# Kernel tuning notes

Hardware: AMD Instinct MI355X
Metric: run time of the kernel (lower is better)

Reference implementation:

```python
import jax, jax.numpy as jnp
import numpy as np

HEADS = 16
KV_HEADS = 4
DIM_HEAD = 64
DIM = 1024
B, N = 2, 2048


def setup_inputs() -> dict:
    key = jax.random.key(0)
    k1, k2, k3 = jax.random.split(key, 3)
    x = jax.random.normal(k1, (B, N, DIM), dtype=jnp.float32)
    Wq = jax.random.normal(k2, (DIM, HEADS * DIM_HEAD), dtype=jnp.float32) / np.sqrt(DIM)
    Wkv = jax.random.normal(k3, (DIM, 2 * KV_HEADS * DIM_HEAD), dtype=jnp.float32) / np.sqrt(DIM)
    k_scale = jnp.ones((HEADS, 1, DIM_HEAD), dtype=jnp.float32)
    return {"x": x, "Wq": Wq, "Wkv": Wkv, "k_scale": k_scale}


def reference(x, Wq, Wkv, k_scale):
    b, n, _ = x.shape
    g = HEADS // KV_HEADS  # query heads per kv head
    scale = DIM_HEAD ** -0.5
    # fused qkv projections (no bias)
    q = (x @ Wq).reshape(b, n, HEADS, DIM_HEAD)
    kv = x @ Wkv
    k, v = jnp.split(kv, 2, axis=-1)
    k = k.reshape(b, n, KV_HEADS, DIM_HEAD).transpose(0, 2, 1, 3)  # b k n d
    v = v.reshape(b, n, KV_HEADS, DIM_HEAD).transpose(0, 2, 1, 3)  # b k n d
    # group query heads: b, kv_heads, g, n, d
    qg = q.transpose(0, 2, 1, 3).reshape(b, KV_HEADS, g, n, DIM_HEAD)
    # per-query-head k scale, applied to the group-broadcast k (qk-norm)
    ks = k_scale.reshape(KV_HEADS, g, 1, DIM_HEAD)
    kk = k[:, :, None, :, :] * ks  # b k g n d
    dots = jnp.einsum('bkgid,bkgjd->bkgij', qg, kk) * scale
    attn = jax.nn.softmax(dots, axis=-1)
    out = jnp.einsum('bkgij,bkjd->bkgid', attn, v)  # v broadcast over g
    out = out.reshape(b, HEADS, n, DIM_HEAD).transpose(0, 2, 1, 3).reshape(b, n, HEADS * DIM_HEAD)
    return out
```

## Files before the change

### kernel.cpp

```cpp
#include <hip/hip_runtime.h>
#include <stdint.h>
#include <math.h>

typedef __attribute__((ext_vector_type(8))) __bf16 bf16x8;
typedef __attribute__((ext_vector_type(4))) float f32x4;
typedef __attribute__((ext_vector_type(16))) float f32x16;

__device__ __forceinline__ uint32_t f32_to_bf16_rne(float f) {
  union { float f; uint32_t u; } v; v.f = f;
  return (v.u + 0x7FFFu + ((v.u >> 16) & 1u)) >> 16;
}

__device__ __forceinline__ uint32_t cvt_pk_bf16(float lo, float hi) {
  uint32_t r;
  asm("v_cvt_pk_bf16_f32 %0, %1, %2" : "=v"(r) : "v"(lo), "v"(hi));
  return r;
}

__device__ __forceinline__ void gld16(void* lds, const void* g) {
  __builtin_amdgcn_global_load_lds(
      (__attribute__((address_space(1))) void*)(g),
      (__attribute__((address_space(3))) void*)(lds), 16, 0, 0);
}

__device__ __forceinline__ f32x4 mfma16(bf16x8 a, bf16x8 b, f32x4 c) {
  return __builtin_amdgcn_mfma_f32_16x16x32_bf16(a, b, c, 0, 0, 0);
}
__device__ __forceinline__ f32x16 mfma32(bf16x8 a, bf16x8 b, f32x16 c) {
  return __builtin_amdgcn_mfma_f32_32x32x16_bf16(a, b, c, 0, 0, 0);
}

#define LOG2E 1.44269504088896340736f

__global__ __launch_bounds__(256) void k_convert_x(const float* __restrict__ x,
                                                   uint16_t* __restrict__ xb) {
  int i = blockIdx.x * 256 + threadIdx.x;
  const float4* xv = (const float4*)x;
  float4 a = xv[2 * i], b2 = xv[2 * i + 1];
  uint32_t w0 = f32_to_bf16_rne(a.x) | (f32_to_bf16_rne(a.y) << 16);
  uint32_t w1 = f32_to_bf16_rne(a.z) | (f32_to_bf16_rne(a.w) << 16);
  uint32_t w2 = f32_to_bf16_rne(b2.x) | (f32_to_bf16_rne(b2.y) << 16);
  uint32_t w3 = f32_to_bf16_rne(b2.z) | (f32_to_bf16_rne(b2.w) << 16);
  ((uint4*)xb)[i] = make_uint4(w0, w1, w2, w3);
}

__global__ __launch_bounds__(256) void k_convert_w(const float* __restrict__ wq,
                                                   const float* __restrict__ wkv,
                                                   uint16_t* __restrict__ wt) {
  __shared__ float tile[64][65];
  int c0 = blockIdx.x * 64, k0 = blockIdx.y * 64;
  int t = threadIdx.x;
  int col = t & 63, rq = t >> 6;
#pragma unroll
  for (int rr = 0; rr < 16; rr++) {
    int r = rr * 4 + rq;
    int c = c0 + col;
    float v = (c < 1024) ? wq[(uint64_t)(k0 + r) * 1024 + c]
                         : wkv[(uint64_t)(k0 + r) * 512 + (c - 1024)];
    tile[r][col] = v;
  }
  __syncthreads();
#pragma unroll
  for (int rr = 0; rr < 16; rr++) {
    int a = rr * 4 + rq;
    wt[(uint64_t)(c0 + a) * 1024 + k0 + col] = (uint16_t)f32_to_bf16_rne(tile[col][a]);
  }
}

__global__ __launch_bounds__(256, 3) void k_proj_gemm(
    const uint16_t* __restrict__ xb, const uint16_t* __restrict__ wt,
    const float* __restrict__ kscale, uint16_t* __restrict__ q_ws,
    uint16_t* __restrict__ k_ws, uint16_t* __restrict__ vt_ws) {
  __shared__ __align__(16) uint16_t As[2][128 * 32];
  __shared__ __align__(16) uint16_t Bs[2][64 * 32];
  int t = threadIdx.x;
  int w = t >> 6, l = t & 63;
  int lq = l & 15, lg = l >> 4;
  int m0 = blockIdx.x * 128, n0 = blockIdx.y * 64;
  int wr = w >> 1, wc = w & 1;
  f32x4 acc[4][2] = {};

  auto stage = [&](int buf, int k0) {
#pragma unroll
    for (int j = 0; j < 2; j++) {
      int tt = j * 256 + t;
      int r = tt >> 2, s = tt & 3;
      int sl = s ^ ((r >> 1) & 3);
      gld16((char*)&As[buf][0] + (j * 256 + w * 64) * 16,
            xb + (uint64_t)(m0 + r) * 1024 + k0 + sl * 8);
    }
    {
      int r = t >> 2, s = t & 3;
      int sl = s ^ ((r >> 1) & 3);
      gld16((char*)&Bs[buf][0] + (w * 64) * 16,
            wt + (uint64_t)(n0 + r) * 1024 + k0 + sl * 8);
    }
  };

  stage(0, 0);
  asm volatile("s_waitcnt vmcnt(0)" ::: "memory");
  __builtin_amdgcn_s_barrier();
  int cur = 0;
  for (int k0 = 0; k0 < 1024; k0 += 32) {
    if (k0 + 32 < 1024) stage(cur ^ 1, k0 + 32);
    bf16x8 af[4], bfr[2];
#pragma unroll
    for (int m = 0; m < 4; m++) {
      int r = wr * 64 + m * 16 + lq;
      int s = lg ^ ((r >> 1) & 3);
      af[m] = *(const bf16x8*)(&As[cur][r * 32 + s * 8]);
    }
#pragma unroll
    for (int n = 0; n < 2; n++) {
      int r = wc * 32 + n * 16 + lq;
      int s = lg ^ ((r >> 1) & 3);
      bfr[n] = *(const bf16x8*)(&Bs[cur][r * 32 + s * 8]);
    }
    __builtin_amdgcn_s_setprio(1);
#pragma unroll
    for (int m = 0; m < 4; m++)
#pragma unroll
      for (int n = 0; n < 2; n++)
        acc[m][n] = mfma16(af[m], bfr[n], acc[m][n]);
    __builtin_amdgcn_s_setprio(0);
    asm volatile("s_waitcnt vmcnt(0) lgkmcnt(0)" ::: "memory");
    __builtin_amdgcn_s_barrier();
    cur ^= 1;
  }

#pragma unroll
  for (int m = 0; m < 4; m++)
#pragma unroll
    for (int n = 0; n < 2; n++)
#pragma unroll
      for (int jj = 0; jj < 4; jj++) {
        int row = m0 + wr * 64 + m * 16 + 4 * lg + jj;
        int col = n0 + wc * 32 + n * 16 + lq;
        float val = acc[m][n][jj];
        int b = row >> 11, nn = row & 2047;
        if (col < 1024) {
          val *= kscale[col] * 0.125f * LOG2E;
          q_ws[((uint64_t)((b * 16 + (col >> 6)) * 2048 + nn)) * 64 + (col & 63)] =
              (uint16_t)f32_to_bf16_rne(val);
        } else if (col < 1280) {
          int kvh = (col - 1024) >> 6;
          k_ws[((uint64_t)((b * 4 + kvh) * 2048 + nn)) * 64 + (col & 63)] =
              (uint16_t)f32_to_bf16_rne(val);
        } else {
          int kvh = (col - 1280) >> 6;
          vt_ws[((uint64_t)((b * 4 + kvh) * 64 + (col & 63))) * 2048 + nn] =
              (uint16_t)f32_to_bf16_rne(val);
        }
      }
}

__global__ __launch_bounds__(256, 2) void k_attn(const uint16_t* __restrict__ q_ws,
                                                 const uint16_t* __restrict__ k_ws,
                                                 const uint16_t* __restrict__ vt_ws,
                                                 float* __restrict__ out) {
  __shared__ __align__(16) uint16_t Ks[2][64 * 64];
  __shared__ __align__(16) uint16_t Vs[2][64 * 64];

  int t = threadIdx.x, w = t >> 6, l = t & 63;
  int lr = l & 31, hi = l >> 5;
  int blk = blockIdx.x;
  int c = blk & 7, j = blk >> 3;
  int b = c >> 2, kvh = c & 3;
  int h = kvh * 4 + (j >> 4), qb = j & 15;

  const uint16_t* Qb = q_ws + (uint64_t)(b * 16 + h) * 2048 * 64;
  const uint16_t* Kb = k_ws + (uint64_t)(b * 4 + kvh) * 2048 * 64;
  const uint16_t* Vb = vt_ws + (uint64_t)(b * 4 + kvh) * 64 * 2048;
  int qrow0 = qb * 128 + w * 32;

  bf16x8 qfrag[4];
#pragma unroll
  for (int m = 0; m < 4; m++)
    qfrag[m] = *(const bf16x8*)(Qb + (uint64_t)(qrow0 + lr) * 64 + m * 16 + hi * 8);

  f32x16 oacc[2] = {};
  float l_run = 0.f;

  auto stageKV = [&](int buf, int kb) {
#pragma unroll
    for (int jj = 0; jj < 2; jj++) {
      int tt = jj * 256 + t;
      int sr = tt >> 3, ss = tt & 7;
      int ssl = ss ^ (sr & 7);
      gld16((char*)&Ks[buf][0] + (jj * 256 + w * 64) * 16,
            Kb + (uint64_t)(kb + sr) * 64 + ssl * 8);
      gld16((char*)&Vs[buf][0] + (jj * 256 + w * 64) * 16,
            Vb + (uint64_t)sr * 2048 + kb + ssl * 8);
    }
  };

  stageKV(0, 0);
  asm volatile("s_waitcnt vmcnt(0)" ::: "memory");
  __builtin_amdgcn_s_barrier();
  int cur = 0;

  for (int kb = 0; kb < 2048; kb += 64) {
    if (kb + 64 < 2048) stageKV(cur ^ 1, kb + 64);

    f32x16 Tacc[2] = {};
    __builtin_amdgcn_s_setprio(1);
#pragma unroll
    for (int st = 0; st < 2; st++) {
      int krow = st * 32 + lr;
#pragma unroll
      for (int m = 0; m < 4; m++) {
        int sl = (2 * m + hi) ^ (lr & 7);
        bf16x8 kf = *(const bf16x8*)(&Ks[cur][krow * 64 + sl * 8]);
        Tacc[st] = mfma32(kf, qfrag[m], Tacc[st]);
      }
    }
    __builtin_amdgcn_s_setprio(0);

    float p[32];
#pragma unroll
    for (int e = 0; e < 16; e++) {
      p[e] = __builtin_amdgcn_exp2f(Tacc[0][e]);
      p[16 + e] = __builtin_amdgcn_exp2f(Tacc[1][e]);
    }
    float sm[8];
#pragma unroll
    for (int i = 0; i < 8; i++)
      sm[i] = (p[4 * i] + p[4 * i + 1]) + (p[4 * i + 2] + p[4 * i + 3]);
    float ls = ((sm[0] + sm[1]) + (sm[2] + sm[3])) + ((sm[4] + sm[5]) + (sm[6] + sm[7]));
    ls += __shfl_xor(ls, 32);
    l_run += ls;

    bf16x8 pa[4];
#pragma unroll
    for (int s = 0; s < 4; s++) {
      int base = (s >> 1) * 16 + (s & 1) * 8;
      uint32_t wlo0 = cvt_pk_bf16(p[base + 0], p[base + 1]);
      uint32_t wlo1 = cvt_pk_bf16(p[base + 2], p[base + 3]);
      uint32_t whi0 = cvt_pk_bf16(p[base + 4], p[base + 5]);
      uint32_t whi1 = cvt_pk_bf16(p[base + 6], p[base + 7]);
      uint32_t send0 = hi ? wlo0 : whi0;
      uint32_t send1 = hi ? wlo1 : whi1;
      uint32_t recv0 = (uint32_t)__shfl_xor((int)send0, 32);
      uint32_t recv1 = (uint32_t)__shfl_xor((int)send1, 32);
      union { uint32_t u[4]; bf16x8 v; } pu;
      pu.u[0] = hi ? recv0 : wlo0;
      pu.u[1] = hi ? recv1 : wlo1;
      pu.u[2] = hi ? whi0 : recv0;
      pu.u[3] = hi ? whi1 : recv1;
      pa[s] = pu.v;
    }

    __builtin_amdgcn_s_setprio(1);
#pragma unroll
    for (int dd = 0; dd < 2; dd++) {
      int vrow = dd * 32 + lr;
#pragma unroll
      for (int s = 0; s < 4; s++) {
        int sl = (2 * s + hi) ^ (lr & 7);
        bf16x8 vf = *(const bf16x8*)(&Vs[cur][vrow * 64 + sl * 8]);
        oacc[dd] = mfma32(pa[s], vf, oacc[dd]);
      }
    }
    __builtin_amdgcn_s_setprio(0);

    asm volatile("s_waitcnt vmcnt(0) lgkmcnt(0)" ::: "memory");
    __builtin_amdgcn_s_barrier();
    cur ^= 1;
  }

  float inv = 1.0f / l_run;
#pragma unroll
  for (int r = 0; r < 16; r++) {
    int qr = (r & 3) + 8 * (r >> 2) + 4 * hi;
    float iv = __shfl(inv, qr);
    float* orow = out + (uint64_t)(b * 2048 + qrow0 + qr) * 1024 + h * 64 + lr;
    orow[0] = oacc[0][r] * iv;
    orow[32] = oacc[1][r] * iv;
  }
}

extern "C" void kernel_launch(void* const* d_in, const int* in_sizes, int n_in,
                              void* d_out, int out_size, void* d_ws, size_t ws_size,
                              hipStream_t stream) {
  const float* x = (const float*)d_in[0];
  const float* wq = (const float*)d_in[1];
  const float* wkv = (const float*)d_in[2];
  const float* kscale = (const float*)d_in[3];
  float* out = (float*)d_out;
  char* ws = (char*)d_ws;
  uint16_t* xb = (uint16_t*)(ws);
  uint16_t* wt = (uint16_t*)(ws + (8ull << 20));
  uint16_t* q_ws = (uint16_t*)(ws + (11ull << 20));
  uint16_t* k_ws = (uint16_t*)(ws + (19ull << 20));
  uint16_t* vt_ws = (uint16_t*)(ws + (21ull << 20));

  k_convert_x<<<2048, 256, 0, stream>>>(x, xb);
  k_convert_w<<<dim3(24, 16), 256, 0, stream>>>(wq, wkv, wt);
  k_proj_gemm<<<dim3(32, 24), 256, 0, stream>>>(xb, wt, kscale, q_ws, k_ws, vt_ws);
  k_attn<<<512, 256, 0, stream>>>(q_ws, k_ws, vt_ws, out);
}
```

Before: 85.70 us.

## Split attention KV range across two wave groups and prelay K/V in fragment order

The projection GEMM now writes K and V into a layout already ordered as MFMA fragments, so the attention kernel can load each fragment with a plain contiguous 16-byte read per lane instead of using swizzled addressing. The attention block doubles to 512 threads. Each half of the block processes half of the 2048 keys, and the partial outputs and row sums are combined through shared memory at the end. This gives more waves per query tile to hide latency, at the cost of a reduction step, 64KB of LDS per block, and possibly lower block occupancy.

```diff
diff --git a/kernel.cpp b/kernel.cpp
--- a/kernel.cpp
+++ b/kernel.cpp
@@ -70,7 +70,7 @@
 __global__ __launch_bounds__(256, 3) void k_proj_gemm(
     const uint16_t* __restrict__ xb, const uint16_t* __restrict__ wt,
     const float* __restrict__ kscale, uint16_t* __restrict__ q_ws,
-    uint16_t* __restrict__ k_ws, uint16_t* __restrict__ vt_ws) {
+    uint16_t* __restrict__ kf_ws, uint16_t* __restrict__ vf_ws) {
   __shared__ __align__(16) uint16_t As[2][128 * 32];
   __shared__ __align__(16) uint16_t Bs[2][64 * 32];
   int t = threadIdx.x;
@@ -144,34 +144,43 @@
               (uint16_t)f32_to_bf16_rne(val);
         } else if (col < 1280) {
           int kvh = (col - 1024) >> 6;
-          k_ws[((uint64_t)((b * 4 + kvh) * 2048 + nn)) * 64 + (col & 63)] =
+          int d = col & 63;
+          int kt = nn >> 6, st = (nn >> 5) & 1, lrr = nn & 31;
+          int mm = d >> 4, hh = (d >> 3) & 1, el = d & 7;
+          kf_ws[(uint64_t)(b * 4 + kvh) * 131072 +
+                (uint64_t)((((kt * 8 + st * 4 + mm) * 64) + hh * 32 + lrr) * 8 + el)] =
               (uint16_t)f32_to_bf16_rne(val);
         } else {
           int kvh = (col - 1280) >> 6;
-          vt_ws[((uint64_t)((b * 4 + kvh) * 64 + (col & 63))) * 2048 + nn] =
+          int d = col & 63;
+          int kt = nn >> 6, nl = nn & 63;
+          int ss = nl >> 4, hh = (nl >> 3) & 1, el = nl & 7;
+          int dd = d >> 5, lrr = d & 31;
+          vf_ws[(uint64_t)(b * 4 + kvh) * 131072 +
+                (uint64_t)((((kt * 8 + dd * 4 + ss) * 64) + hh * 32 + lrr) * 8 + el)] =
               (uint16_t)f32_to_bf16_rne(val);
         }
       }
 }
 
-__global__ __launch_bounds__(256, 2) void k_attn(const uint16_t* __restrict__ q_ws,
-                                                 const uint16_t* __restrict__ k_ws,
-                                                 const uint16_t* __restrict__ vt_ws,
+__global__ __launch_bounds__(512, 4) void k_attn(const uint16_t* __restrict__ q_ws,
+                                                 const uint16_t* __restrict__ kf_ws,
+                                                 const uint16_t* __restrict__ vf_ws,
                                                  float* __restrict__ out) {
-  __shared__ __align__(16) uint16_t Ks[2][64 * 64];
-  __shared__ __align__(16) uint16_t Vs[2][64 * 64];
+  __shared__ __align__(16) char smem[65536];
 
   int t = threadIdx.x, w = t >> 6, l = t & 63;
   int lr = l & 31, hi = l >> 5;
+  int wq = w & 3, half = w >> 2;
   int blk = blockIdx.x;
   int c = blk & 7, j = blk >> 3;
   int b = c >> 2, kvh = c & 3;
   int h = kvh * 4 + (j >> 4), qb = j & 15;
 
   const uint16_t* Qb = q_ws + (uint64_t)(b * 16 + h) * 2048 * 64;
-  const uint16_t* Kb = k_ws + (uint64_t)(b * 4 + kvh) * 2048 * 64;
-  const uint16_t* Vb = vt_ws + (uint64_t)(b * 4 + kvh) * 64 * 2048;
-  int qrow0 = qb * 128 + w * 32;
+  const uint16_t* Kb = kf_ws + (uint64_t)(b * 4 + kvh) * 131072;
+  const uint16_t* Vb = vf_ws + (uint64_t)(b * 4 + kvh) * 131072;
+  int qrow0 = qb * 128 + wq * 32;
 
   bf16x8 qfrag[4];
 #pragma unroll
@@ -181,39 +190,38 @@
   f32x16 oacc[2] = {};
   float l_run = 0.f;
 
-  auto stageKV = [&](int buf, int kb) {
-#pragma unroll
-    for (int jj = 0; jj < 2; jj++) {
-      int tt = jj * 256 + t;
-      int sr = tt >> 3, ss = tt & 7;
-      int ssl = ss ^ (sr & 7);
-      gld16((char*)&Ks[buf][0] + (jj * 256 + w * 64) * 16,
-            Kb + (uint64_t)(kb + sr) * 64 + ssl * 8);
-      gld16((char*)&Vs[buf][0] + (jj * 256 + w * 64) * 16,
-            Vb + (uint64_t)sr * 2048 + kb + ssl * 8);
+  char* KsBase = smem + half * 32768;
+  char* VsBase = smem + half * 32768 + 16384;
+
+  auto stageKV = [&](int buf, int kt) {
+#pragma unroll
+    for (int ii = 0; ii < 2; ii++) {
+      int idx = wq * 2 + ii;
+      gld16(KsBase + buf * 8192 + idx * 1024, Kb + (uint64_t)(kt * 8 + idx) * 512 + l * 8);
+      gld16(VsBase + buf * 8192 + idx * 1024, Vb + (uint64_t)(kt * 8 + idx) * 512 + l * 8);
     }
   };
 
-  stageKV(0, 0);
+  int kt0 = half * 16;
+  stageKV(0, kt0);
   asm volatile("s_waitcnt vmcnt(0)" ::: "memory");
   __builtin_amdgcn_s_barrier();
   int cur = 0;
 
-  for (int kb = 0; kb < 2048; kb += 64) {
-    if (kb + 64 < 2048) stageKV(cur ^ 1, kb + 64);
+  for (int it = 0; it < 16; it++) {
+    if (it + 1 < 16) stageKV(cur ^ 1, kt0 + it + 1);
+    const uint16_t* Ksc = (const uint16_t*)(KsBase + cur * 8192);
+    const uint16_t* Vsc = (const uint16_t*)(VsBase + cur * 8192);
 
     f32x16 Tacc[2] = {};
     __builtin_amdgcn_s_setprio(1);
 #pragma unroll
-    for (int st = 0; st < 2; st++) {
-      int krow = st * 32 + lr;
+    for (int st = 0; st < 2; st++)
 #pragma unroll
       for (int m = 0; m < 4; m++) {
-        int sl = (2 * m + hi) ^ (lr & 7);
-        bf16x8 kf = *(const bf16x8*)(&Ks[cur][krow * 64 + sl * 8]);
+        bf16x8 kf = *(const bf16x8*)(Ksc + (st * 4 + m) * 512 + l * 8);
         Tacc[st] = mfma32(kf, qfrag[m], Tacc[st]);
       }
-    }
     __builtin_amdgcn_s_setprio(0);
 
     float p[32];
@@ -252,15 +260,12 @@
 
     __builtin_amdgcn_s_setprio(1);
 #pragma unroll
-    for (int dd = 0; dd < 2; dd++) {
-      int vrow = dd * 32 + lr;
+    for (int dd = 0; dd < 2; dd++)
 #pragma unroll
       for (int s = 0; s < 4; s++) {
-        int sl = (2 * s + hi) ^ (lr & 7);
-        bf16x8 vf = *(const bf16x8*)(&Vs[cur][vrow * 64 + sl * 8]);
+        bf16x8 vf = *(const bf16x8*)(Vsc + (dd * 4 + s) * 512 + l * 8);
         oacc[dd] = mfma32(pa[s], vf, oacc[dd]);
       }
-    }
     __builtin_amdgcn_s_setprio(0);
 
     asm volatile("s_waitcnt vmcnt(0) lgkmcnt(0)" ::: "memory");
@@ -268,14 +273,31 @@
     cur ^= 1;
   }
 
-  float inv = 1.0f / l_run;
-#pragma unroll
-  for (int r = 0; r < 16; r++) {
-    int qr = (r & 3) + 8 * (r >> 2) + 4 * hi;
-    float iv = __shfl(inv, qr);
-    float* orow = out + (uint64_t)(b * 2048 + qrow0 + qr) * 1024 + h * 64 + lr;
-    orow[0] = oacc[0][r] * iv;
-    orow[32] = oacc[1][r] * iv;
+  float* exch = (float*)smem;
+  float* exl = (float*)(smem + 32768);
+  if (half == 1) {
+#pragma unroll
+    for (int r = 0; r < 16; r++) {
+      int qr = (r & 3) + 8 * (r >> 2) + 4 * hi;
+      exch[wq * 2048 + qr * 64 + lr] = oacc[0][r];
+      exch[wq * 2048 + qr * 64 + 32 + lr] = oacc[1][r];
+    }
+    if (hi == 0) exl[wq * 32 + lr] = l_run;
+  }
+  __syncthreads();
+  if (half == 0) {
+    l_run += exl[wq * 32 + lr];
+    float inv = 1.0f / l_run;
+#pragma unroll
+    for (int r = 0; r < 16; r++) {
+      int qr = (r & 3) + 8 * (r >> 2) + 4 * hi;
+      float iv = __shfl(inv, qr);
+      float o0 = oacc[0][r] + exch[wq * 2048 + qr * 64 + lr];
+      float o1 = oacc[1][r] + exch[wq * 2048 + qr * 64 + 32 + lr];
+      float* orow = out + (uint64_t)(b * 2048 + qrow0 + qr) * 1024 + h * 64 + lr;
+      orow[0] = o0 * iv;
+      orow[32] = o1 * iv;
+    }
   }
 }
 
@@ -291,11 +313,11 @@
   uint16_t* xb = (uint16_t*)(ws);
   uint16_t* wt = (uint16_t*)(ws + (8ull << 20));
   uint16_t* q_ws = (uint16_t*)(ws + (11ull << 20));
-  uint16_t* k_ws = (uint16_t*)(ws + (19ull << 20));
-  uint16_t* vt_ws = (uint16_t*)(ws + (21ull << 20));
+  uint16_t* kf_ws = (uint16_t*)(ws + (19ull << 20));
+  uint16_t* vf_ws = (uint16_t*)(ws + (21ull << 20));
 
   k_convert_x<<<2048, 256, 0, stream>>>(x, xb);
   k_convert_w<<<dim3(24, 16), 256, 0, stream>>>(wq, wkv, wt);
-  k_proj_gemm<<<dim3(32, 24), 256, 0, stream>>>(xb, wt, kscale, q_ws, k_ws, vt_ws);
-  k_attn<<<512, 256, 0, stream>>>(q_ws, k_ws, vt_ws, out);
-}
+  k_proj_gemm<<<dim3(32, 24), 256, 0, stream>>>(xb, wt, kscale, q_ws, kf_ws, vf_ws);
+  k_attn<<<512, 512, 0, stream>>>(q_ws, kf_ws, vf_ws, out);
+}
```

New measurement: 81.64 us. -4.7%, faster.
